# Kernel optimization log

Hardware: AMD Instinct MI355X
Metric: run time of the kernel (lower is better)

The kernel has to match this reference:

```python
import jax, jax.numpy as jnp
import numpy as np

B, U, K, N = 1024, 2048, 2, 2  # batch, num_units, num_k_splits, num_n_splits


def setup_inputs() -> dict:
    key = jax.random.key(0)
    k1, k2, k3, k4 = jax.random.split(key, 4)
    x = jax.random.normal(k1, (B, U), dtype=jnp.float32)
    h = jax.random.normal(k2, (B, U), dtype=jnp.float32)
    c = jax.random.normal(k3, (B, U), dtype=jnp.float32)
    # W[i, j] is the per-device weight of shape [2U/K, 4U/N] (device d = i*N + j)
    W = jax.random.normal(k4, (K, N, 2 * U // K, 4 * U // N), dtype=jnp.float32) * 0.02
    return {"x": x, "h": h, "c": c, "W": W}


def reference(x, h, c, W):
    Bs, Us = x.shape
    Ks, Ns = W.shape[0], W.shape[1]
    # Split x and h into K column blocks of width U/K and pair them per k-split:
    # xh_i = concat(x_i, h_i)  -> [K, B, 2U/K]
    xk = x.reshape(Bs, Ks, Us // Ks).transpose(1, 0, 2)
    hk = h.reshape(Bs, Ks, Us // Ks).transpose(1, 0, 2)
    xh = jnp.concatenate([xk, hk], axis=2)
    # ParallelGEMM: ifgo_j = sum_i xh_i @ W[i, j]  -> [B, N, 4U/N]
    ifgo = jnp.einsum('kbd,kndf->bnf', xh, W)
    # Gate fusion: split the 4U/N columns into i, f, g, o of width U/N each
    i_g, f_g, g_g, o_g = jnp.split(ifgo, 4, axis=2)
    i_g = jax.nn.sigmoid(i_g)
    f_g = jax.nn.sigmoid(f_g)
    o_g = jax.nn.sigmoid(o_g)
    g_g = jnp.tanh(g_g)
    cn = c.reshape(Bs, Ns, Us // Ns)  # c held as N blocks of width U/N
    new_c = f_g * cn + i_g * g_g
    new_h = o_g * jnp.tanh(new_c)
    # Ring all-concat just reassembles the full hidden state
    return new_h.reshape(Bs, Us), new_c.reshape(Bs, Us)
```

## Files before the change

kernel.cpp:

```cpp
#include <hip/hip_runtime.h>
#include <hip/hip_bf16.h>


typedef short bf16x8 __attribute__((ext_vector_type(8)));
typedef float f32x4  __attribute__((ext_vector_type(4)));

__device__ __forceinline__ unsigned pkcvt(float a, float b) {
#if defined(__has_builtin) && __has_builtin(__builtin_amdgcn_cvt_pk_bf16_f32)
  typedef __bf16 bf16x2_t __attribute__((ext_vector_type(2)));
  bf16x2_t r = __builtin_amdgcn_cvt_pk_bf16_f32(a, b);
  union { bf16x2_t v; unsigned u; } cv; cv.v = r;
  return cv.u;
#else
  unsigned ua = __float_as_uint(a), ub = __float_as_uint(b);
  ua = (ua + 0x7fffu + ((ua >> 16) & 1u)) >> 16;
  ub = (ub + 0x7fffu + ((ub >> 16) & 1u)) & 0xffff0000u;
  return ua | ub;
#endif
}

union pk8 { unsigned u[4]; bf16x8 v; };

__device__ __forceinline__ void gl_lds16(const void* g, void* l) {
  __builtin_amdgcn_global_load_lds(
      (const __attribute__((address_space(1))) unsigned*)g,
      (__attribute__((address_space(3))) unsigned*)l, 16, 0, 0);
}

__global__ __launch_bounds__(256)
void prep_xh(const float* __restrict__ x, const float* __restrict__ h, void* wsAv)
{
  const int gid = blockIdx.x * 256 + threadIdx.x;
  const int row = gid >> 9;
  const int r9  = gid & 511;
  const int kt  = r9 >> 3;
  const int pc  = r9 & 7;
  const int lc  = pc ^ (row & 7);
  const int k0  = kt * 64 + lc * 8;
  const int blk = k0 >> 10;
  const float* src = ((blk & 1) ? h : x) + row * 2048 + (blk >> 1) * 1024 + (k0 & 1023);
  const float4 p0 = ((const float4*)src)[0];
  const float4 p1 = ((const float4*)src)[1];
  pk8 o;
  o.u[0] = pkcvt(p0.x, p0.y); o.u[1] = pkcvt(p0.z, p0.w);
  o.u[2] = pkcvt(p1.x, p1.y); o.u[3] = pkcvt(p1.z, p1.w);
  *(bf16x8*)((char*)wsAv + (size_t)row * 8192 + kt * 128 + pc * 16) = o.v;
}

__global__ __launch_bounds__(256)
void prep_w(const float* __restrict__ W, void* wsBv)
{
  __shared__ short Ls[64 * 72];
  const int t  = threadIdx.x;
  const int pb = blockIdx.x;
  const int kT = pb & 63;
  const int cT = (pb >> 6) & 63;
  const int n  = pb >> 12;
  const int c0 = cT * 64;
  const int k0 = kT * 64;
  const int kq = k0 >> 11;
  const int krow0 = k0 & 2047;

  const int c_l  = t & 63;
  const int kgrp = t >> 6;
  const int c    = c0 + c_l;
  const int col  = (c & 3) * 1024 + (c >> 2);
  const float* src = W + ((size_t)(kq * 2 + n) * 2048 + krow0 + kgrp * 16) * 4096 + col;
  #pragma unroll
  for (int i = 0; i < 16; i += 2) {
    const float a = src[(size_t)i * 4096];
    const float b = src[(size_t)(i + 1) * 4096];
    *(unsigned*)&Ls[c_l * 72 + kgrp * 16 + i] = pkcvt(a, b);
  }
  __syncthreads();
  #pragma unroll
  for (int half = 0; half < 2; ++half) {
    const int j   = t + half * 256;
    const int cl2 = j >> 3;
    const int pc  = j & 7;
    const int cc  = c0 + cl2;
    const int lc2 = pc ^ (cc & 7);
    const bf16x8 v = *(const bf16x8*)&Ls[cl2 * 72 + lc2 * 8];
    *(bf16x8*)((char*)wsBv + ((size_t)(n * 4096 + cc) * 8192) + (size_t)(k0 + pc * 8) * 2) = v;
  }
}

__global__ __launch_bounds__(256, 3)
void lstm_mm(const void* wsAv, const void* wsBv,
             const float* __restrict__ cin, float* __restrict__ out)
{
  __shared__ short As[128 * 64];
  __shared__ short Bs[128 * 64];

  const int tid  = threadIdx.x;
  const int lane = tid & 63;
  const int wid  = tid >> 6;
  const int wr   = wid >> 1;
  const int wc   = wid & 1;

  const int bid     = blockIdx.x;
  const int rowblk  = bid >> 6;
  const int colblk  = bid & 63;
  const int n       = colblk >> 5;
  const int u0      = (colblk & 31) * 32;
  const int rowbase = rowblk * 128;

  const int am   = lane & 15;
  const int quad = lane >> 4;
  const int rA   = lane >> 3;
  const int pcA  = lane & 7;

  const char* wsA = (const char*)wsAv;
  const char* wsB = (const char*)wsBv;
  const size_t aRowBase = (size_t)(rowbase + wid * 32) * 8192;
  const size_t bRowBase = (size_t)(n * 4096 + 4 * u0 + wid * 32) * 8192;

  f32x4 acc[4][4];
  const f32x4 zero = {0.f, 0.f, 0.f, 0.f};
  #pragma unroll
  for (int i = 0; i < 4; ++i)
    #pragma unroll
    for (int j = 0; j < 4; ++j) acc[i][j] = zero;

  for (int kt = 0; kt < 64; ++kt) {
    __syncthreads();
    #pragma unroll
    for (int q = 0; q < 4; ++q) {
      gl_lds16(wsA + aRowBase + (size_t)(q * 8 + rA) * 8192 + kt * 128 + pcA * 16,
               &As[(wid * 32 + q * 8) * 64]);
      gl_lds16(wsB + bRowBase + (size_t)(q * 8 + rA) * 8192 + kt * 128 + pcA * 16,
               &Bs[(wid * 32 + q * 8) * 64]);
    }
    __syncthreads();

    #pragma unroll
    for (int s = 0; s < 2; ++s) {
      const int sw = ((s * 4 + quad) ^ (am & 7)) * 8;
      bf16x8 af[4], bfr[4];
      #pragma unroll
      for (int tm = 0; tm < 4; ++tm)
        af[tm] = *(const bf16x8*)&As[(wr * 64 + tm * 16 + am) * 64 + sw];
      #pragma unroll
      for (int tn = 0; tn < 4; ++tn)
        bfr[tn] = *(const bf16x8*)&Bs[(wc * 64 + tn * 16 + am) * 64 + sw];
      #pragma unroll
      for (int tm = 0; tm < 4; ++tm)
        #pragma unroll
        for (int tn = 0; tn < 4; ++tn)
          acc[tm][tn] = __builtin_amdgcn_mfma_f32_16x16x32_bf16(
              af[tm], bfr[tn], acc[tm][tn], 0, 0, 0);
    }
  }

  const int BU   = 1024 * 2048;
  const int g    = lane & 3;
  const int base = lane & ~3;
  #pragma unroll
  for (int tn = 0; tn < 4; ++tn) {
    const int cil = wc * 64 + tn * 16 + am;
    const int col = n * 1024 + u0 + (cil >> 2);
    #pragma unroll
    for (int tm = 0; tm < 4; ++tm) {
      const int brow0 = rowbase + wr * 64 + tm * 16 + quad * 4;
      #pragma unroll
      for (int r = 0; r < 4; ++r) {
        const int brow = brow0 + r;
        const float val = acc[tm][tn][r];
        const float xs  = (g == 2) ? 2.f * val : val;
        const float sg  = 1.f / (1.f + __expf(-xs));
        const float act = (g == 2) ? (2.f * sg - 1.f) : sg;
        const float ig = __shfl(act, base + 0, 64);
        const float fg = __shfl(act, base + 1, 64);
        const float gg = __shfl(act, base + 2, 64);
        const float og = __shfl(act, base + 3, 64);
        const float cold = cin[brow * 2048 + col];
        const float nc = fg * cold + ig * gg;
        const float th = 1.f - 2.f / (1.f + __expf(2.f * nc));
        const float nh = og * th;
        if (g == 0) out[brow * 2048 + col]      = nh;
        if (g == 1) out[BU + brow * 2048 + col] = nc;
      }
    }
  }
}

__global__ __launch_bounds__(512, 4)
void lstm_fused_fb(const float* __restrict__ x, const float* __restrict__ h,
                   const float* __restrict__ cin, const float* __restrict__ W,
                   float* __restrict__ out)
{
  __shared__ short As[128 * 64];
  __shared__ short Bs[128 * 64];
  const int tid  = threadIdx.x;
  const int lane = tid & 63;
  const int wid  = tid >> 6;
  const int wr   = wid >> 2;
  const int wq   = wid & 3;
  const int bid     = blockIdx.x;
  const int rowblk  = bid >> 6;
  const int colblk  = bid & 63;
  const int n       = colblk >> 5;
  const int u0      = (colblk & 31) * 32;
  const int rowbase = rowblk * 128;
  const int ar = tid >> 2;
  const int aq = tid & 3;
  const int bc   = tid & 127;
  const int bgt  = bc & 3;
  const int bu   = bc >> 2;
  const int kgrp = tid >> 7;
  const int gcol = bgt * 1024 + u0 + bu;
  const int am   = lane & 15;
  const int quad = lane >> 4;

  f32x4 acc[4][2];
  const f32x4 zero = {0.f, 0.f, 0.f, 0.f};
  #pragma unroll
  for (int i = 0; i < 4; ++i)
    #pragma unroll
    for (int j = 0; j < 2; ++j) acc[i][j] = zero;

  float4 areg[4];
  float  breg[16];
  auto load_tiles = [&](int kt) {
    const int blk = kt >> 4;
    const float* asrc = (blk & 1) ? h : x;
    const int cb = (blk >> 1) * 1024 + (kt & 15) * 64;
    const float4* p = (const float4*)(asrc + (rowbase + ar) * 2048 + cb + aq * 16);
    #pragma unroll
    for (int q = 0; q < 4; ++q) areg[q] = p[q];
    const int kq = kt >> 5;
    const float* wp = W + ((kq * 2 + n) * 2048 + (kt & 31) * 64 + kgrp * 16) * 4096 + gcol;
    #pragma unroll
    for (int j = 0; j < 16; ++j) breg[j] = wp[j * 4096];
  };
  load_tiles(0);
  for (int kt = 0; kt < 64; ++kt) {
    bf16x8 aw[2];
    {
      pk8 p0, p1;
      p0.u[0] = pkcvt(areg[0].x, areg[0].y); p0.u[1] = pkcvt(areg[0].z, areg[0].w);
      p0.u[2] = pkcvt(areg[1].x, areg[1].y); p0.u[3] = pkcvt(areg[1].z, areg[1].w);
      p1.u[0] = pkcvt(areg[2].x, areg[2].y); p1.u[1] = pkcvt(areg[2].z, areg[2].w);
      p1.u[2] = pkcvt(areg[3].x, areg[3].y); p1.u[3] = pkcvt(areg[3].z, areg[3].w);
      aw[0] = p0.v; aw[1] = p1.v;
    }
    bf16x8 bw[2];
    {
      pk8 q0, q1;
      #pragma unroll
      for (int j = 0; j < 4; ++j) {
        q0.u[j] = pkcvt(breg[2 * j],     breg[2 * j + 1]);
        q1.u[j] = pkcvt(breg[8 + 2 * j], breg[8 + 2 * j + 1]);
      }
      bw[0] = q0.v; bw[1] = q1.v;
    }
    __syncthreads();
    #pragma unroll
    for (int hh = 0; hh < 2; ++hh)
      *(bf16x8*)&As[ar * 64 + (((aq * 2 + hh) ^ (ar & 7)) * 8)] = aw[hh];
    #pragma unroll
    for (int hh = 0; hh < 2; ++hh)
      *(bf16x8*)&Bs[bc * 64 + (((kgrp * 2 + hh) ^ (bc & 7)) * 8)] = bw[hh];
    __syncthreads();
    if (kt < 63) load_tiles(kt + 1);
    #pragma unroll
    for (int s = 0; s < 2; ++s) {
      const int sw = ((s * 4 + quad) ^ (am & 7)) * 8;
      bf16x8 af[4], bfr[2];
      #pragma unroll
      for (int tm = 0; tm < 4; ++tm)
        af[tm] = *(const bf16x8*)&As[(wr * 64 + tm * 16 + am) * 64 + sw];
      #pragma unroll
      for (int tn = 0; tn < 2; ++tn)
        bfr[tn] = *(const bf16x8*)&Bs[(wq * 32 + tn * 16 + am) * 64 + sw];
      #pragma unroll
      for (int tm = 0; tm < 4; ++tm)
        #pragma unroll
        for (int tn = 0; tn < 2; ++tn)
          acc[tm][tn] = __builtin_amdgcn_mfma_f32_16x16x32_bf16(
              af[tm], bfr[tn], acc[tm][tn], 0, 0, 0);
    }
  }
  const int BU   = 1024 * 2048;
  const int g    = lane & 3;
  const int base = lane & ~3;
  #pragma unroll
  for (int tn = 0; tn < 2; ++tn) {
    const int cil = wq * 32 + tn * 16 + am;
    const int col = n * 1024 + u0 + (cil >> 2);
    #pragma unroll
    for (int tm = 0; tm < 4; ++tm) {
      const int brow0 = rowbase + wr * 64 + tm * 16 + quad * 4;
      #pragma unroll
      for (int r = 0; r < 4; ++r) {
        const int brow = brow0 + r;
        const float val = acc[tm][tn][r];
        const float xs  = (g == 2) ? 2.f * val : val;
        const float sg  = 1.f / (1.f + __expf(-xs));
        const float act = (g == 2) ? (2.f * sg - 1.f) : sg;
        const float ig = __shfl(act, base + 0, 64);
        const float fg = __shfl(act, base + 1, 64);
        const float gg = __shfl(act, base + 2, 64);
        const float og = __shfl(act, base + 3, 64);
        const float cold = cin[brow * 2048 + col];
        const float nc = fg * cold + ig * gg;
        const float th = 1.f - 2.f / (1.f + __expf(2.f * nc));
        const float nh = og * th;
        if (g == 0) out[brow * 2048 + col]      = nh;
        if (g == 1) out[BU + brow * 2048 + col] = nc;
      }
    }
  }
}

extern "C" void kernel_launch(void* const* d_in, const int* in_sizes, int n_in,
                              void* d_out, int out_size, void* d_ws, size_t ws_size,
                              hipStream_t stream) {
  const float* x = (const float*)d_in[0];
  const float* h = (const float*)d_in[1];
  const float* c = (const float*)d_in[2];
  const float* W = (const float*)d_in[3];
  float* out = (float*)d_out;

  const size_t WSA_BYTES = (size_t)1024 * 4096 * 2;
  const size_t WSB_BYTES = (size_t)2 * 4096 * 4096 * 2;
  if (ws_size >= WSA_BYTES + WSB_BYTES) {
    char* wsA = (char*)d_ws;
    char* wsB = (char*)d_ws + WSA_BYTES;
    prep_xh<<<dim3(2048), dim3(256), 0, stream>>>(x, h, wsA);
    prep_w<<<dim3(8192), dim3(256), 0, stream>>>(W, wsB);
    lstm_mm<<<dim3(512), dim3(256), 0, stream>>>(wsA, wsB, c, out);
  } else {
    lstm_fused_fb<<<dim3(512), dim3(512), 0, stream>>>(x, h, c, W, out);
  }
}
```

Measured before the change: 322.9 us.

## Merge xh and weight prep kernels with vectorized float4 weight reads

Combines the activation and weight bf16 conversion kernels into a single launch split by block index. The weight path now reads float4 vectors along contiguous columns, covering 64 rows by 256 columns per block in a padded LDS tile, and gathers scalar bf16 values from LDS to write the transposed, gate-interleaved layout. This targets the strided scalar global reads of the old weight prep, which dominate the cost of converting the 64MB weight tensor, and also saves one launch. The price is more scalar LDS reads and a larger shared-memory footprint per block.

After: 313.4 us. -2.9%, faster.

```diff
diff --git a/kernel.cpp b/kernel.cpp
--- a/kernel.cpp
+++ b/kernel.cpp
@@ -28,60 +28,73 @@
 }
 
 __global__ __launch_bounds__(256)
-void prep_xh(const float* __restrict__ x, const float* __restrict__ h, void* wsAv)
+void prep_all(const float* __restrict__ x, const float* __restrict__ h,
+              const float* __restrict__ W, void* wsAv, void* wsBv)
 {
-  const int gid = blockIdx.x * 256 + threadIdx.x;
-  const int row = gid >> 9;
-  const int r9  = gid & 511;
-  const int kt  = r9 >> 3;
-  const int pc  = r9 & 7;
-  const int lc  = pc ^ (row & 7);
-  const int k0  = kt * 64 + lc * 8;
-  const int blk = k0 >> 10;
-  const float* src = ((blk & 1) ? h : x) + row * 2048 + (blk >> 1) * 1024 + (k0 & 1023);
-  const float4 p0 = ((const float4*)src)[0];
-  const float4 p1 = ((const float4*)src)[1];
-  pk8 o;
-  o.u[0] = pkcvt(p0.x, p0.y); o.u[1] = pkcvt(p0.z, p0.w);
-  o.u[2] = pkcvt(p1.x, p1.y); o.u[3] = pkcvt(p1.z, p1.w);
-  *(bf16x8*)((char*)wsAv + (size_t)row * 8192 + kt * 128 + pc * 16) = o.v;
-}
-
-__global__ __launch_bounds__(256)
-void prep_w(const float* __restrict__ W, void* wsBv)
-{
-  __shared__ short Ls[64 * 72];
-  const int t  = threadIdx.x;
-  const int pb = blockIdx.x;
-  const int kT = pb & 63;
-  const int cT = (pb >> 6) & 63;
-  const int n  = pb >> 12;
-  const int c0 = cT * 64;
-  const int k0 = kT * 64;
-  const int kq = k0 >> 11;
-  const int krow0 = k0 & 2047;
-
-  const int c_l  = t & 63;
-  const int kgrp = t >> 6;
-  const int c    = c0 + c_l;
-  const int col  = (c & 3) * 1024 + (c >> 2);
-  const float* src = W + ((size_t)(kq * 2 + n) * 2048 + krow0 + kgrp * 16) * 4096 + col;
-  #pragma unroll
-  for (int i = 0; i < 16; i += 2) {
-    const float a = src[(size_t)i * 4096];
-    const float b = src[(size_t)(i + 1) * 4096];
-    *(unsigned*)&Ls[c_l * 72 + kgrp * 16 + i] = pkcvt(a, b);
-  }
-  __syncthreads();
-  #pragma unroll
-  for (int half = 0; half < 2; ++half) {
-    const int j   = t + half * 256;
-    const int cl2 = j >> 3;
-    const int pc  = j & 7;
-    const int cc  = c0 + cl2;
-    const int lc2 = pc ^ (cc & 7);
-    const bf16x8 v = *(const bf16x8*)&Ls[cl2 * 72 + lc2 * 8];
-    *(bf16x8*)((char*)wsBv + ((size_t)(n * 4096 + cc) * 8192) + (size_t)(k0 + pc * 8) * 2) = v;
+  __shared__ short Ls[64 * 258];
+  const int t   = threadIdx.x;
+  const int bid = blockIdx.x;
+
+  if (bid < 2048) {
+    const int utile = bid & 15;
+    const int ktile = (bid >> 4) & 63;
+    const int n     = bid >> 10;
+    const int u0    = utile * 64;
+    const int k0    = ktile * 64;
+    const int kq    = k0 >> 11;
+    const int krow0 = k0 & 2047;
+
+    const int g    = t >> 6;
+    const int l15  = t & 15;
+    const int rsel = (t >> 4) & 3;
+    const float* wbase = W + ((size_t)(kq * 2 + n) * 2048 + krow0) * 4096
+                           + g * 1024 + u0 + l15 * 4;
+    #pragma unroll 4
+    for (int i = 0; i < 16; ++i) {
+      const int kk = i * 4 + rsel;
+      const float4 v = *(const float4*)(wbase + (size_t)kk * 4096);
+      const int ad = kk * 258 + g * 64 + l15 * 4;
+      *(unsigned*)&Ls[ad]     = pkcvt(v.x, v.y);
+      *(unsigned*)&Ls[ad + 2] = pkcvt(v.z, v.w);
+    }
+    __syncthreads();
+
+    const int cg = t >> 3;
+    const int pc = t & 7;
+    char* outb = (char*)wsBv + (size_t)(n * 4096 + u0 * 4) * 8192
+               + (size_t)k0 * 2 + pc * 16;
+    #pragma unroll
+    for (int j2 = 0; j2 < 8; ++j2) {
+      const int c_l  = j2 * 32 + cg;
+      const int gg   = c_l & 3;
+      const int uloc = c_l >> 2;
+      const int lc   = pc ^ (c_l & 7);
+      const int base = lc * 8 * 258 + gg * 64 + uloc;
+      pk8 o;
+      #pragma unroll
+      for (int q = 0; q < 4; ++q) {
+        const unsigned s0 = (unsigned short)Ls[base + (2 * q)     * 258];
+        const unsigned s1 = (unsigned short)Ls[base + (2 * q + 1) * 258];
+        o.u[q] = s0 | (s1 << 16);
+      }
+      *(bf16x8*)(outb + (size_t)c_l * 8192) = o.v;
+    }
+  } else {
+    const int gid = (bid - 2048) * 256 + t;
+    const int row = gid >> 9;
+    const int r9  = gid & 511;
+    const int kt  = r9 >> 3;
+    const int pcx = r9 & 7;
+    const int lcx = pcx ^ (row & 7);
+    const int kk0 = kt * 64 + lcx * 8;
+    const int blk = kk0 >> 10;
+    const float* src = ((blk & 1) ? h : x) + row * 2048 + (blk >> 1) * 1024 + (kk0 & 1023);
+    const float4 p0 = ((const float4*)src)[0];
+    const float4 p1 = ((const float4*)src)[1];
+    pk8 o;
+    o.u[0] = pkcvt(p0.x, p0.y); o.u[1] = pkcvt(p0.z, p0.w);
+    o.u[2] = pkcvt(p1.x, p1.y); o.u[3] = pkcvt(p1.z, p1.w);
+    *(bf16x8*)((char*)wsAv + (size_t)row * 8192 + kt * 128 + pcx * 16) = o.v;
   }
 }
 
@@ -327,8 +340,7 @@
   if (ws_size >= WSA_BYTES + WSB_BYTES) {
     char* wsA = (char*)d_ws;
     char* wsB = (char*)d_ws + WSA_BYTES;
-    prep_xh<<<dim3(2048), dim3(256), 0, stream>>>(x, h, wsA);
-    prep_w<<<dim3(8192), dim3(256), 0, stream>>>(W, wsB);
+    prep_all<<<dim3(4096), dim3(256), 0, stream>>>(x, h, W, wsA, wsB);
     lstm_mm<<<dim3(512), dim3(256), 0, stream>>>(wsA, wsB, c, out);
   } else {
     lstm_fused_fb<<<dim3(512), dim3(512), 0, stream>>>(x, h, c, W, out);
```
